# Performance work log

Hardware: AMD Instinct MI355X
Metric: run time of the kernel (lower is better)

## Reference

```python
import jax, jax.numpy as jnp
import numpy as np

# Hard-coded joint groups from GLAGCNModule (num_joints=25)
GROUPS = [
    list(range(25)),                    # full_body
    [0, 1, 2, 3, 4, 5, 6, 7, 8],        # upper_body
    [0, 9, 10, 11, 12, 13, 14],         # lower_body
    [6, 7, 8, 12, 13, 14],              # left_limbs
    [3, 4, 5, 9, 10, 11],               # right_limbs
]

B, N, D_IN, D_HID = 8192, 25, 256, 512


def setup_inputs() -> dict:
    key = jax.random.key(0)
    ks = jax.random.split(key, 7)
    # Xavier-uniform-ish scales for the stacked per-group GCN weights
    s1 = float(np.sqrt(6.0 / (D_IN + D_HID)))
    s2 = float(np.sqrt(6.0 / (D_HID + D_IN)))
    return {
        "x": jax.random.normal(ks[0], (B, N, D_IN), dtype=jnp.float32),
        "adj": jax.random.uniform(ks[1], (B, N, N), dtype=jnp.float32),
        "W1": jax.random.uniform(ks[2], (5, D_IN, D_HID), jnp.float32, -s1, s1),
        "b1": jnp.zeros((5, D_HID), dtype=jnp.float32),
        "W2": jax.random.uniform(ks[3], (5, D_HID, D_IN), jnp.float32, -s2, s2),
        "b2": jnp.zeros((5, D_IN), dtype=jnp.float32),
        "fusion_w": jnp.ones((5,), dtype=jnp.float32),
    }


def _graph_conv(x, adj, W, b):
    """x: (B,n,din), adj: (B,n,n) -> (B,n,dout). Sym-normalized GCN + ReLU."""
    n = adj.shape[-1]
    A = adj + jnp.eye(n, dtype=adj.dtype)          # add self-loops
    deg = jnp.sum(A, axis=-1)                      # (B,n)
    deg_safe = jnp.where(deg == 0, 1.0, deg)
    dinv = jnp.where(deg == 0, 0.0, deg_safe ** -0.5)  # inf -> 0 as in torch
    norm_adj = dinv[:, :, None] * A * dinv[:, None, :]  # D^-1/2 A D^-1/2
    support = jnp.einsum('bnd,de->bne', x, W)
    out = jnp.einsum('bnm,bme->bne', norm_adj, support) + b
    return jax.nn.relu(out)


def reference(x, adj, W1, b1, W2, b2, fusion_w):
    norm_w = jax.nn.softmax(fusion_w)
    fused = jnp.zeros_like(x)
    for g, idx_list in enumerate(GROUPS):
        idx = jnp.asarray(idx_list)
        x_g = x[:, idx, :]                      # (B, ng, D)
        adj_g = adj[:, idx][:, :, idx]          # (B, ng, ng) gather of sub-adjacency
        h = _graph_conv(x_g, adj_g, W1[g], b1[g])
        out_g = _graph_conv(h, adj_g, W2[g], b2[g])
        # scatter back to full joint set, weighted fuse
        fused = fused.at[:, idx, :].add(norm_w[g] * out_g)
    return fused
```

## Files before the change

### kernel.cpp

```cpp
#include <hip/hip_runtime.h>
#include <hip/hip_bf16.h>
#include <stdint.h>

typedef short bf16x8 __attribute__((ext_vector_type(8)));
typedef float f32x4 __attribute__((ext_vector_type(4)));
typedef unsigned short u16;
typedef unsigned int u32;

#define B_TOT 8192
#define NN 25

__device__ __forceinline__ u16 f2bf(float f) {
  u32 u = __float_as_uint(f);
  u32 r = (u + 0x7fffu + ((u >> 16) & 1u)) >> 16;
  return (u16)r;
}
__device__ __forceinline__ float bf2f(u16 h) {
  return __uint_as_float(((u32)h) << 16);
}

__device__ __constant__ int d_IDXT[5][25] = {
  {0,1,2,3,4,5,6,7,8,9,10,11,12,13,14,15,16,17,18,19,20,21,22,23,24},
  {0,1,2,3,4,5,6,7,8, 0,0,0,0,0,0,0,0,0,0,0,0,0,0,0,0},
  {0,9,10,11,12,13,14, 0,0,0,0,0,0,0,0,0,0,0,0,0,0,0,0,0,0},
  {6,7,8,12,13,14, 0,0,0,0,0,0,0,0,0,0,0,0,0,0,0,0,0,0,0},
  {3,4,5,9,10,11, 0,0,0,0,0,0,0,0,0,0,0,0,0,0,0,0,0,0,0}
};
__device__ __constant__ int d_NG[5]    = {25, 9, 7, 6, 6};
__device__ __constant__ int d_BW[5]    = {1, 3, 4, 5, 5};
__device__ __constant__ int d_PREFN[5] = {0, 25, 34, 41, 47};
__device__ __constant__ int d_GCNT[25] = {3,2,2,3,3,3,3,3,3,3,3,3,3,3,3,1,1,1,1,1,1,1,1,1,1};
__device__ __constant__ signed char d_GG[25][3] = {
  {0,1,2},{0,1,0},{0,1,0},{0,1,4},{0,1,4},{0,1,4},{0,1,3},{0,1,3},{0,1,3},
  {0,2,4},{0,2,4},{0,2,4},{0,2,3},{0,2,3},{0,2,3},
  {0,0,0},{0,0,0},{0,0,0},{0,0,0},{0,0,0},{0,0,0},{0,0,0},{0,0,0},{0,0,0},{0,0,0}};
__device__ __constant__ signed char d_GP[25][3] = {
  {0,0,0},{1,1,0},{2,2,0},{3,3,0},{4,4,1},{5,5,2},{6,6,0},{7,7,1},{8,8,2},
  {9,1,3},{10,2,4},{11,3,5},{12,4,3},{13,5,4},{14,6,5},
  {15,0,0},{16,0,0},{17,0,0},{18,0,0},{19,0,0},{20,0,0},{21,0,0},{22,0,0},{23,0,0},{24,0,0}};

__global__ __launch_bounds__(256) void prep_kernel(const float* __restrict__ W1,
                                                   const float* __restrict__ W2,
                                                   u16* __restrict__ w1t,
                                                   u16* __restrict__ w2t) {
  __shared__ float tile[32][33];
  int bid = blockIdx.x, t = threadIdx.x;
  const float* src; u16* dst; int R, C, tr, tc;
  if (bid < 640) {
    int g = bid >> 7, tI = bid & 127;
    R = 256; C = 512; tr = tI >> 4; tc = tI & 15;
    src = W1 + (size_t)g * 131072; dst = w1t + (size_t)g * 131072;
  } else {
    int b2 = bid - 640; int g = b2 >> 7, tI = b2 & 127;
    R = 512; C = 256; tr = tI >> 3; tc = tI & 7;
    src = W2 + (size_t)g * 131072; dst = w2t + (size_t)g * 131072;
  }
  for (int e = t; e < 1024; e += 256) {
    int r = e >> 5, c = e & 31;
    tile[r][c] = src[(size_t)(tr * 32 + r) * C + tc * 32 + c];
  }
  __syncthreads();
  for (int e = t; e < 1024; e += 256) {
    int c = e >> 5, r = e & 31;
    dst[(size_t)(tc * 32 + c) * R + tr * 32 + r] = f2bf(tile[r][c]);
  }
}

struct __align__(16) SMem {
  u16 xs[120 * 256];
  u16 wt[128 * 64];
  u16 bd[128 * 32];
  u16 u[256 * 128];
  float b1s[512];
  float b2s[256];
  float dinv[500];
  u16 rowLUT[128];
};
static_assert(sizeof(SMem) <= 160 * 1024, "LDS overflow");

__global__ __launch_bounds__(512) void gcn_group_kernel(
    const float* __restrict__ x, const float* __restrict__ adj,
    const float* __restrict__ b1, const float* __restrict__ b2,
    const float* __restrict__ fw,
    const u16* __restrict__ w1t, const u16* __restrict__ w2t,
    u16* __restrict__ wsout, float* __restrict__ out, int use_ws) {
  __shared__ SMem sm;
  int bid = blockIdx.x;
  int g, tile;
  if (bid < 2048)      { g = 0; tile = bid; }
  else if (bid < 2731) { g = 1; tile = bid - 2048; }
  else if (bid < 3243) { g = 2; tile = bid - 2731; }
  else if (bid < 3653) { g = 3; tile = bid - 3243; }
  else                 { g = 4; tile = bid - 3653; }
  const int ng = d_NG[g], bw = d_BW[g];
  const int tb = bw * 4;
  const int tb0 = tile * tb;
  const int tid = threadIdx.x;
  const int lane = tid & 63, wid = tid >> 6, wm = wid >> 2, wn = wid & 3;

  if (tid < 128) {
    int w = tid >> 5, off = tid & 31;
    int j = off / ng, i = off - j * ng;
    int valid = (j < bw) ? 1 : 0;
    int bl = w * bw + j;
    sm.rowLUT[tid] = (u16)((valid << 15) | ((bl & 31) << 5) | i);
  }
  sm.b1s[tid] = b1[g * 512 + tid];
  if (tid < 256) sm.b2s[tid] = b2[g * 256 + tid];

  const int nrows = tb * ng;
  for (int cid = tid; cid < nrows * 64; cid += 512) {
    int r = cid >> 6, c4 = cid & 63;
    int bl = r / ng, i = r - bl * ng;
    int b = tb0 + bl;
    float4 v = make_float4(0.f, 0.f, 0.f, 0.f);
    if (b < B_TOT) {
      const float* p = x + ((size_t)b * NN + d_IDXT[g][i]) * 256 + c4 * 4;
      v = *(const float4*)p;
    }
    u32 p0 = (u32)f2bf(v.x) | ((u32)f2bf(v.y) << 16);
    u32 p1 = (u32)f2bf(v.z) | ((u32)f2bf(v.w) << 16);
    u32 off = (u32)r * 512u + (((u32)c4 * 8u) ^ (((u32)r & 7u) << 4));
    *(uint2*)((char*)sm.xs + off) = make_uint2(p0, p1);
  }

  if (tid < nrows) {
    int bl = tid / ng, i = tid - bl * ng;
    int b = tb0 + bl;
    float s = 1.0f;
    if (b < B_TOT) {
      const float* ar = adj + ((size_t)b * NN + d_IDXT[g][i]) * NN;
      for (int j2 = 0; j2 < ng; ++j2) s += ar[d_IDXT[g][j2]];
    }
    sm.dinv[bl * 25 + i] = (s > 0.f) ? rsqrtf(s) : 0.f;
  }
  __syncthreads();

  u32 arow[4], aswz[4];
#pragma unroll
  for (int m = 0; m < 4; ++m) {
    int r = wm * 64 + m * 16 + (lane & 15);
    u16 lut = sm.rowLUT[r];
    int rxs = 0;
    if (lut & 0x8000) rxs = ((lut >> 5) & 31) * ng + (lut & 31);
    arow[m] = (u32)rxs * 512u;
    aswz[m] = ((u32)rxs & 7u) << 4;
  }

  for (int e = tid; e < 4096; e += 512) {
    int r = e >> 5, c = e & 31;
    u16 lr = sm.rowLUT[r];
    u16 lc = sm.rowLUT[(r & ~31) | c];
    float val = 0.f;
    int blr = (lr >> 5) & 31, ir = lr & 31;
    int blc = (lc >> 5) & 31, ic = lc & 31;
    int b = tb0 + blr;
    if ((lr >> 15) && (lc >> 15) && blr == blc && b < B_TOT) {
      float a = adj[((size_t)b * NN + d_IDXT[g][ir]) * NN + d_IDXT[g][ic]] +
                (ir == ic ? 1.f : 0.f);
      val = sm.dinv[blr * 25 + ir] * a * sm.dinv[blr * 25 + ic];
    }
    u32 off = (u32)r * 64u + (((u32)c * 2u) ^ (((u32)r & 3u) << 4));
    *(u16*)((char*)sm.bd + off) = f2bf(val);
  }

  float wg = 0.2f;
  if (!use_ws) {
    float a0 = fw[0], a1 = fw[1], a2 = fw[2], a3 = fw[3], a4 = fw[4];
    float mx = fmaxf(fmaxf(fmaxf(a0, a1), fmaxf(a2, a3)), a4);
    float e0 = __expf(a0 - mx), e1 = __expf(a1 - mx), e2 = __expf(a2 - mx),
          e3 = __expf(a3 - mx), e4 = __expf(a4 - mx);
    float es[5] = {e0, e1, e2, e3, e4};
    wg = es[g] / (e0 + e1 + e2 + e3 + e4);
  }

  f32x4 zero4 = {0.f, 0.f, 0.f, 0.f};
  f32x4 accO[4][2][2];
#pragma unroll
  for (int m = 0; m < 4; ++m)
#pragma unroll
    for (int a = 0; a < 2; ++a)
#pragma unroll
      for (int bq = 0; bq < 2; ++bq) accO[m][a][bq] = zero4;

#pragma unroll 1
  for (int c = 0; c < 4; ++c) {
    f32x4 accS[4][2];
#pragma unroll
    for (int m = 0; m < 4; ++m) { accS[m][0] = zero4; accS[m][1] = zero4; }

    for (int kt = 0; kt < 4; ++kt) {
#pragma unroll
      for (int it = 0; it < 2; ++it) {
        int cid = tid + it * 512;
        int row = cid >> 3, p = cid & 7;
        const u16* src = w1t + (size_t)(g * 512 + c * 128 + row) * 256 + kt * 64 + p * 8;
        uint4 v = *(const uint4*)src;
        u32 off = (u32)row * 128u + (((u32)p * 16u) ^ (((u32)row & 7u) << 4));
        *(uint4*)((char*)sm.wt + off) = v;
      }
      __syncthreads();
#pragma unroll
      for (int ks = 0; ks < 2; ++ks) {
        u32 colb = (u32)(kt * 128 + ks * 64) + (((u32)lane >> 4) << 4);
        bf16x8 afr[4];
#pragma unroll
        for (int m = 0; m < 4; ++m)
          afr[m] = *(const bf16x8*)((const char*)sm.xs + arow[m] + (colb ^ aswz[m]));
#pragma unroll
        for (int nf = 0; nf < 2; ++nf) {
          int nl = (wn * 2 + nf) * 16 + (lane & 15);
          u32 boff = (u32)nl * 128u +
                     (((u32)(ks * 64) + (((u32)lane >> 4) << 4)) ^ (((u32)nl & 7u) << 4));
          bf16x8 bfr = *(const bf16x8*)((const char*)sm.wt + boff);
#pragma unroll
          for (int m = 0; m < 4; ++m)
            accS[m][nf] = __builtin_amdgcn_mfma_f32_16x16x32_bf16(afr[m], bfr, accS[m][nf], 0, 0, 0);
        }
      }
      __syncthreads();
    }

#pragma unroll
    for (int m = 0; m < 4; ++m) {
      int mrow0 = wm * 64 + m * 16 + ((lane >> 4) << 2);
#pragma unroll
      for (int nf = 0; nf < 2; ++nf) {
        int f = (wn * 2 + nf) * 16 + (lane & 15);
        u32 p0 = (u32)f2bf(accS[m][nf][0]) | ((u32)f2bf(accS[m][nf][1]) << 16);
        u32 p1 = (u32)f2bf(accS[m][nf][2]) | ((u32)f2bf(accS[m][nf][3]) << 16);
        u32 off = (u32)f * 256u + (((u32)mrow0 * 2u) ^ (((u32)f & 7u) << 4));
        *(uint2*)((char*)sm.u + off) = make_uint2(p0, p1);
      }
    }
    __syncthreads();

#pragma unroll
    for (int m = 0; m < 4; ++m) {
      int mf = wm * 4 + m, win = mf >> 1;
      int br = mf * 16 + (lane & 15);
      u32 aoff = (u32)br * 64u + (((((u32)lane >> 4) << 4)) ^ (((u32)br & 3u) << 4));
      bf16x8 abd = *(const bf16x8*)((const char*)sm.bd + aoff);
#pragma unroll
      for (int nf = 0; nf < 2; ++nf) {
        int f = (wn * 2 + nf) * 16 + (lane & 15);
        u32 boff = (u32)f * 256u +
                   (((u32)(win * 64) + (((u32)lane >> 4) << 4)) ^ (((u32)f & 7u) << 4));
        bf16x8 bfr = *(const bf16x8*)((const char*)sm.u + boff);
        f32x4 d = zero4;
        d = __builtin_amdgcn_mfma_f32_16x16x32_bf16(abd, bfr, d, 0, 0, 0);
        float bb = sm.b1s[c * 128 + f];
#pragma unroll
        for (int r2 = 0; r2 < 4; ++r2) {
          int mrow = mf * 16 + ((lane >> 4) << 2) + r2;
          float hv = d[r2] + bb;
          hv = hv > 0.f ? hv : 0.f;
          u32 hoff = 32768u + (u32)mrow * 256u + (((u32)f * 2u) ^ (((u32)mrow & 7u) << 4));
          *(u16*)((char*)sm.u + hoff) = f2bf(hv);
        }
      }
    }
    __syncthreads();

#pragma unroll
    for (int nh = 0; nh < 2; ++nh) {
#pragma unroll
      for (int kt2 = 0; kt2 < 2; ++kt2) {
#pragma unroll
        for (int it = 0; it < 2; ++it) {
          int cid = tid + it * 512;
          int row = cid >> 3, p = cid & 7;
          const u16* src = w2t + (size_t)(g * 256 + nh * 128 + row) * 512 +
                           c * 128 + kt2 * 64 + p * 8;
          uint4 v = *(const uint4*)src;
          u32 off = (u32)row * 128u + (((u32)p * 16u) ^ (((u32)row & 7u) << 4));
          *(uint4*)((char*)sm.wt + off) = v;
        }
        __syncthreads();
#pragma unroll
        for (int ks = 0; ks < 2; ++ks) {
          bf16x8 afr[4];
#pragma unroll
          for (int m = 0; m < 4; ++m) {
            int mrow = wm * 64 + m * 16 + (lane & 15);
            u32 aoff = 32768u + (u32)mrow * 256u +
                       (((u32)(kt2 * 128 + ks * 64) + (((u32)lane >> 4) << 4)) ^
                        (((u32)mrow & 7u) << 4));
            afr[m] = *(const bf16x8*)((const char*)sm.u + aoff);
          }
#pragma unroll
          for (int nf = 0; nf < 2; ++nf) {
            int nl = (wn * 2 + nf) * 16 + (lane & 15);
            u32 boff = (u32)nl * 128u +
                       (((u32)(ks * 64) + (((u32)lane >> 4) << 4)) ^ (((u32)nl & 7u) << 4));
            bf16x8 bfr = *(const bf16x8*)((const char*)sm.wt + boff);
#pragma unroll
            for (int m = 0; m < 4; ++m)
              accO[m][nh][nf] =
                  __builtin_amdgcn_mfma_f32_16x16x32_bf16(afr[m], bfr, accO[m][nh][nf], 0, 0, 0);
          }
        }
        __syncthreads();
      }
    }
  }

#pragma unroll
  for (int m = 0; m < 4; ++m) {
    int mrow0 = wm * 64 + m * 16 + ((lane >> 4) << 2);
#pragma unroll
    for (int nh = 0; nh < 2; ++nh)
#pragma unroll
      for (int nf = 0; nf < 2; ++nf) {
        int f = nh * 128 + (wn * 2 + nf) * 16 + (lane & 15);
        u32 p0 = (u32)f2bf(accO[m][nh][nf][0]) | ((u32)f2bf(accO[m][nh][nf][1]) << 16);
        u32 p1 = (u32)f2bf(accO[m][nh][nf][2]) | ((u32)f2bf(accO[m][nh][nf][3]) << 16);
        u32 off = (u32)f * 256u + (((u32)mrow0 * 2u) ^ (((u32)f & 7u) << 4));
        *(uint2*)((char*)sm.u + off) = make_uint2(p0, p1);
      }
  }
  __syncthreads();

  u16* wbase = wsout + (size_t)d_PREFN[g] * B_TOT * 256;
#pragma unroll
  for (int m = 0; m < 4; ++m) {
    int mf = wm * 4 + m, win = mf >> 1;
    int br = mf * 16 + (lane & 15);
    u32 aoff = (u32)br * 64u + (((((u32)lane >> 4) << 4)) ^ (((u32)br & 3u) << 4));
    bf16x8 abd = *(const bf16x8*)((const char*)sm.bd + aoff);
#pragma unroll
    for (int q = 0; q < 4; ++q) {
      int f = (wn * 4 + q) * 16 + (lane & 15);
      u32 boff = (u32)f * 256u +
                 (((u32)(win * 64) + (((u32)lane >> 4) << 4)) ^ (((u32)f & 7u) << 4));
      bf16x8 bfr = *(const bf16x8*)((const char*)sm.u + boff);
      f32x4 d = zero4;
      d = __builtin_amdgcn_mfma_f32_16x16x32_bf16(abd, bfr, d, 0, 0, 0);
      float bb = sm.b2s[f];
#pragma unroll
      for (int r2 = 0; r2 < 4; ++r2) {
        int mrow = mf * 16 + ((lane >> 4) << 2) + r2;
        u16 lut = sm.rowLUT[mrow];
        if (!(lut & 0x8000)) continue;
        int bl = (lut >> 5) & 31, i = lut & 31;
        int b = tb0 + bl;
        if (b >= B_TOT) continue;
        float v = d[r2] + bb;
        v = v > 0.f ? v : 0.f;
        if (use_ws) {
          wbase[((size_t)b * ng + i) * 256 + f] = f2bf(v);
        } else {
          float* dst = out + ((size_t)b * NN + d_IDXT[g][i]) * 256 + f;
          __hip_atomic_fetch_add(dst, wg * v, __ATOMIC_RELAXED, __HIP_MEMORY_SCOPE_AGENT);
        }
      }
    }
  }
}

__global__ __launch_bounds__(256) void gather_kernel(const u16* __restrict__ wsout,
                                                     const float* __restrict__ fw,
                                                     float* __restrict__ out) {
  int t = blockIdx.x * 256 + threadIdx.x;
  int b = t / 1600;
  int rem = t - b * 1600;
  int v = rem >> 6;
  int f = (rem & 63) << 2;
  float a0 = fw[0], a1 = fw[1], a2 = fw[2], a3 = fw[3], a4 = fw[4];
  float mx = fmaxf(fmaxf(fmaxf(a0, a1), fmaxf(a2, a3)), a4);
  float e0 = __expf(a0 - mx), e1 = __expf(a1 - mx), e2 = __expf(a2 - mx),
        e3 = __expf(a3 - mx), e4 = __expf(a4 - mx);
  float inv = 1.f / (e0 + e1 + e2 + e3 + e4);
  float w[5] = {e0 * inv, e1 * inv, e2 * inv, e3 * inv, e4 * inv};
  float acc0 = 0.f, acc1 = 0.f, acc2 = 0.f, acc3 = 0.f;
  int cnt = d_GCNT[v];
  for (int k = 0; k < cnt; ++k) {
    int g = d_GG[v][k], pos = d_GP[v][k];
    const u16* p = wsout + (size_t)d_PREFN[g] * B_TOT * 256 +
                   ((size_t)b * d_NG[g] + pos) * 256 + f;
    ushort4 h = *(const ushort4*)p;
    float ww = w[g];
    acc0 += ww * bf2f(h.x);
    acc1 += ww * bf2f(h.y);
    acc2 += ww * bf2f(h.z);
    acc3 += ww * bf2f(h.w);
  }
  *(float4*)(out + (size_t)t * 4) = make_float4(acc0, acc1, acc2, acc3);
}

extern "C" void kernel_launch(void* const* d_in, const int* in_sizes, int n_in,
                              void* d_out, int out_size, void* d_ws, size_t ws_size,
                              hipStream_t stream) {
  const float* x   = (const float*)d_in[0];
  const float* adj = (const float*)d_in[1];
  const float* W1  = (const float*)d_in[2];
  const float* b1  = (const float*)d_in[3];
  const float* W2  = (const float*)d_in[4];
  const float* b2  = (const float*)d_in[5];
  const float* fw  = (const float*)d_in[6];
  float* out = (float*)d_out;
  char* ws = (char*)d_ws;

  u16* w1t   = (u16*)ws;
  u16* w2t   = (u16*)(ws + 1310720);
  u16* wsout = (u16*)(ws + 2621440);
  const size_t need = 2621440ull + 53ull * 8192ull * 256ull * 2ull;
  const int use_ws = (ws_size >= need) ? 1 : 0;

  prep_kernel<<<1280, 256, 0, stream>>>(W1, W2, w1t, w2t);
  if (!use_ws) {
    hipMemsetAsync(out, 0, (size_t)out_size * sizeof(float), stream);
  }
  gcn_group_kernel<<<4063, 512, 0, stream>>>(x, adj, b1, b2, fw, w1t, w2t,
                                             wsout, out, use_ws);
  if (use_ws) {
    gather_kernel<<<51200, 256, 0, stream>>>(wsout, fw, out);
  }
}
```

Baseline: 1.500 ms.

## Load GEMM weight fragments straight from global memory and transpose the adjacency MFMA epilogue

Removes the shared-memory weight tile and the per-k-step barriers. Each lane now loads its W1/W2 bf16 fragments directly from global memory (expected to hit L2) into registers. The block-diagonal adjacency MFMAs are transposed so each lane holds four consecutive features of a single row. This lets bias loads, h stores and output writes be vectorized (float4/uint2), with the row LUT checked once per row. The trade is more global and L2 load traffic and register pressure in exchange for fewer syncs and less LDS use.

```diff
diff --git a/kernel.cpp b/kernel.cpp
--- a/kernel.cpp
+++ b/kernel.cpp
@@ -68,7 +68,6 @@
 
 struct __align__(16) SMem {
   u16 xs[120 * 256];
-  u16 wt[128 * 64];
   u16 bd[128 * 32];
   u16 u[256 * 128];
   float b1s[512];
@@ -183,23 +182,25 @@
 #pragma unroll
       for (int bq = 0; bq < 2; ++bq) accO[m][a][bq] = zero4;
 
+  __syncthreads();
+
 #pragma unroll 1
   for (int c = 0; c < 4; ++c) {
     f32x4 accS[4][2];
 #pragma unroll
     for (int m = 0; m < 4; ++m) { accS[m][0] = zero4; accS[m][1] = zero4; }
 
+#pragma unroll
     for (int kt = 0; kt < 4; ++kt) {
-#pragma unroll
-      for (int it = 0; it < 2; ++it) {
-        int cid = tid + it * 512;
-        int row = cid >> 3, p = cid & 7;
-        const u16* src = w1t + (size_t)(g * 512 + c * 128 + row) * 256 + kt * 64 + p * 8;
-        uint4 v = *(const uint4*)src;
-        u32 off = (u32)row * 128u + (((u32)p * 16u) ^ (((u32)row & 7u) << 4));
-        *(uint4*)((char*)sm.wt + off) = v;
-      }
-      __syncthreads();
+      bf16x8 bfr[2][2];
+#pragma unroll
+      for (int ks = 0; ks < 2; ++ks)
+#pragma unroll
+        for (int nf = 0; nf < 2; ++nf) {
+          int n = c * 128 + (wn * 2 + nf) * 16 + (lane & 15);
+          int k = kt * 64 + ks * 32 + ((lane >> 4) << 3);
+          bfr[ks][nf] = *(const bf16x8*)(w1t + ((size_t)(g * 512 + n) * 256 + k));
+        }
 #pragma unroll
       for (int ks = 0; ks < 2; ++ks) {
         u32 colb = (u32)(kt * 128 + ks * 64) + (((u32)lane >> 4) << 4);
@@ -208,17 +209,11 @@
         for (int m = 0; m < 4; ++m)
           afr[m] = *(const bf16x8*)((const char*)sm.xs + arow[m] + (colb ^ aswz[m]));
 #pragma unroll
-        for (int nf = 0; nf < 2; ++nf) {
-          int nl = (wn * 2 + nf) * 16 + (lane & 15);
-          u32 boff = (u32)nl * 128u +
-                     (((u32)(ks * 64) + (((u32)lane >> 4) << 4)) ^ (((u32)nl & 7u) << 4));
-          bf16x8 bfr = *(const bf16x8*)((const char*)sm.wt + boff);
+        for (int nf = 0; nf < 2; ++nf)
 #pragma unroll
           for (int m = 0; m < 4; ++m)
-            accS[m][nf] = __builtin_amdgcn_mfma_f32_16x16x32_bf16(afr[m], bfr, accS[m][nf], 0, 0, 0);
-        }
-      }
-      __syncthreads();
+            accS[m][nf] = __builtin_amdgcn_mfma_f32_16x16x32_bf16(afr[m], bfr[ks][nf], accS[m][nf], 0, 0, 0);
+      }
     }
 
 #pragma unroll
@@ -237,46 +232,44 @@
 
 #pragma unroll
     for (int m = 0; m < 4; ++m) {
-      int mf = wm * 4 + m, win = mf >> 1;
-      int br = mf * 16 + (lane & 15);
-      u32 aoff = (u32)br * 64u + (((((u32)lane >> 4) << 4)) ^ (((u32)br & 3u) << 4));
-      bf16x8 abd = *(const bf16x8*)((const char*)sm.bd + aoff);
-#pragma unroll
-      for (int nf = 0; nf < 2; ++nf) {
-        int f = (wn * 2 + nf) * 16 + (lane & 15);
-        u32 boff = (u32)f * 256u +
+      int mb = wm * 4 + m, win = mb >> 1;
+      int mrow = mb * 16 + (lane & 15);
+      u32 boff = (u32)mrow * 64u + (((((u32)lane >> 4) << 4)) ^ (((u32)mrow & 3u) << 4));
+      bf16x8 bfr = *(const bf16x8*)((const char*)sm.bd + boff);
+#pragma unroll
+      for (int a = 0; a < 2; ++a) {
+        int f = (wn * 2 + a) * 16 + (lane & 15);
+        u32 aoff = (u32)f * 256u +
                    (((u32)(win * 64) + (((u32)lane >> 4) << 4)) ^ (((u32)f & 7u) << 4));
-        bf16x8 bfr = *(const bf16x8*)((const char*)sm.u + boff);
-        f32x4 d = zero4;
-        d = __builtin_amdgcn_mfma_f32_16x16x32_bf16(abd, bfr, d, 0, 0, 0);
-        float bb = sm.b1s[c * 128 + f];
-#pragma unroll
-        for (int r2 = 0; r2 < 4; ++r2) {
-          int mrow = mf * 16 + ((lane >> 4) << 2) + r2;
-          float hv = d[r2] + bb;
-          hv = hv > 0.f ? hv : 0.f;
-          u32 hoff = 32768u + (u32)mrow * 256u + (((u32)f * 2u) ^ (((u32)mrow & 7u) << 4));
-          *(u16*)((char*)sm.u + hoff) = f2bf(hv);
-        }
+        bf16x8 afr = *(const bf16x8*)((const char*)sm.u + aoff);
+        f32x4 d = __builtin_amdgcn_mfma_f32_16x16x32_bf16(afr, bfr, zero4, 0, 0, 0);
+        int f0 = (wn * 2 + a) * 16 + ((lane >> 4) << 2);
+        float4 bb = *(const float4*)&sm.b1s[c * 128 + f0];
+        float h0 = d[0] + bb.x; h0 = h0 > 0.f ? h0 : 0.f;
+        float h1 = d[1] + bb.y; h1 = h1 > 0.f ? h1 : 0.f;
+        float h2 = d[2] + bb.z; h2 = h2 > 0.f ? h2 : 0.f;
+        float h3 = d[3] + bb.w; h3 = h3 > 0.f ? h3 : 0.f;
+        u32 p0 = (u32)f2bf(h0) | ((u32)f2bf(h1) << 16);
+        u32 p1 = (u32)f2bf(h2) | ((u32)f2bf(h3) << 16);
+        u32 hoff = 32768u + (u32)mrow * 256u + (((u32)f0 * 2u) ^ (((u32)mrow & 7u) << 4));
+        *(uint2*)((char*)sm.u + hoff) = make_uint2(p0, p1);
       }
     }
     __syncthreads();
 
 #pragma unroll
-    for (int nh = 0; nh < 2; ++nh) {
+    for (int nh = 0; nh < 2; ++nh)
 #pragma unroll
       for (int kt2 = 0; kt2 < 2; ++kt2) {
-#pragma unroll
-        for (int it = 0; it < 2; ++it) {
-          int cid = tid + it * 512;
-          int row = cid >> 3, p = cid & 7;
-          const u16* src = w2t + (size_t)(g * 256 + nh * 128 + row) * 512 +
-                           c * 128 + kt2 * 64 + p * 8;
-          uint4 v = *(const uint4*)src;
-          u32 off = (u32)row * 128u + (((u32)p * 16u) ^ (((u32)row & 7u) << 4));
-          *(uint4*)((char*)sm.wt + off) = v;
-        }
-        __syncthreads();
+        bf16x8 bfr2[2][2];
+#pragma unroll
+        for (int ks = 0; ks < 2; ++ks)
+#pragma unroll
+          for (int nf = 0; nf < 2; ++nf) {
+            int n = nh * 128 + (wn * 2 + nf) * 16 + (lane & 15);
+            int k = c * 128 + kt2 * 64 + ks * 32 + ((lane >> 4) << 3);
+            bfr2[ks][nf] = *(const bf16x8*)(w2t + ((size_t)(g * 256 + n) * 512 + k));
+          }
 #pragma unroll
         for (int ks = 0; ks < 2; ++ks) {
           bf16x8 afr[4];
@@ -289,21 +282,16 @@
             afr[m] = *(const bf16x8*)((const char*)sm.u + aoff);
           }
 #pragma unroll
-          for (int nf = 0; nf < 2; ++nf) {
-            int nl = (wn * 2 + nf) * 16 + (lane & 15);
-            u32 boff = (u32)nl * 128u +
-                       (((u32)(ks * 64) + (((u32)lane >> 4) << 4)) ^ (((u32)nl & 7u) << 4));
-            bf16x8 bfr = *(const bf16x8*)((const char*)sm.wt + boff);
+          for (int nf = 0; nf < 2; ++nf)
 #pragma unroll
             for (int m = 0; m < 4; ++m)
               accO[m][nh][nf] =
-                  __builtin_amdgcn_mfma_f32_16x16x32_bf16(afr[m], bfr, accO[m][nh][nf], 0, 0, 0);
-          }
+                  __builtin_amdgcn_mfma_f32_16x16x32_bf16(afr[m], bfr2[ks][nf], accO[m][nh][nf], 0, 0, 0);
         }
-        __syncthreads();
-      }
-    }
-  }
+      }
+  }
+
+  __syncthreads();
 
 #pragma unroll
   for (int m = 0; m < 4; ++m) {
@@ -324,34 +312,39 @@
   u16* wbase = wsout + (size_t)d_PREFN[g] * B_TOT * 256;
 #pragma unroll
   for (int m = 0; m < 4; ++m) {
-    int mf = wm * 4 + m, win = mf >> 1;
-    int br = mf * 16 + (lane & 15);
-    u32 aoff = (u32)br * 64u + (((((u32)lane >> 4) << 4)) ^ (((u32)br & 3u) << 4));
-    bf16x8 abd = *(const bf16x8*)((const char*)sm.bd + aoff);
+    int mb = wm * 4 + m, win = mb >> 1;
+    int mrow = mb * 16 + (lane & 15);
+    u32 boff = (u32)mrow * 64u + (((((u32)lane >> 4) << 4)) ^ (((u32)mrow & 3u) << 4));
+    bf16x8 bfr = *(const bf16x8*)((const char*)sm.bd + boff);
+    u16 lut = sm.rowLUT[mrow];
+    int bl = (lut >> 5) & 31, i = lut & 31;
+    int b = tb0 + bl;
+    bool ok = (lut & 0x8000) && (b < B_TOT);
 #pragma unroll
     for (int q = 0; q < 4; ++q) {
-      int f = (wn * 4 + q) * 16 + (lane & 15);
-      u32 boff = (u32)f * 256u +
+      int fb = wn * 4 + q;
+      int f = fb * 16 + (lane & 15);
+      u32 aoff = (u32)f * 256u +
                  (((u32)(win * 64) + (((u32)lane >> 4) << 4)) ^ (((u32)f & 7u) << 4));
-      bf16x8 bfr = *(const bf16x8*)((const char*)sm.u + boff);
-      f32x4 d = zero4;
-      d = __builtin_amdgcn_mfma_f32_16x16x32_bf16(abd, bfr, d, 0, 0, 0);
-      float bb = sm.b2s[f];
-#pragma unroll
-      for (int r2 = 0; r2 < 4; ++r2) {
-        int mrow = mf * 16 + ((lane >> 4) << 2) + r2;
-        u16 lut = sm.rowLUT[mrow];
-        if (!(lut & 0x8000)) continue;
-        int bl = (lut >> 5) & 31, i = lut & 31;
-        int b = tb0 + bl;
-        if (b >= B_TOT) continue;
-        float v = d[r2] + bb;
-        v = v > 0.f ? v : 0.f;
+      bf16x8 afr = *(const bf16x8*)((const char*)sm.u + aoff);
+      f32x4 d = __builtin_amdgcn_mfma_f32_16x16x32_bf16(afr, bfr, zero4, 0, 0, 0);
+      int f0 = fb * 16 + ((lane >> 4) << 2);
+      float4 bb = *(const float4*)&sm.b2s[f0];
+      float v0 = d[0] + bb.x; v0 = v0 > 0.f ? v0 : 0.f;
+      float v1 = d[1] + bb.y; v1 = v1 > 0.f ? v1 : 0.f;
+      float v2 = d[2] + bb.z; v2 = v2 > 0.f ? v2 : 0.f;
+      float v3 = d[3] + bb.w; v3 = v3 > 0.f ? v3 : 0.f;
+      if (ok) {
         if (use_ws) {
-          wbase[((size_t)b * ng + i) * 256 + f] = f2bf(v);
+          u32 p0 = (u32)f2bf(v0) | ((u32)f2bf(v1) << 16);
+          u32 p1 = (u32)f2bf(v2) | ((u32)f2bf(v3) << 16);
+          *(uint2*)(wbase + ((size_t)b * ng + i) * 256 + f0) = make_uint2(p0, p1);
         } else {
-          float* dst = out + ((size_t)b * NN + d_IDXT[g][i]) * 256 + f;
-          __hip_atomic_fetch_add(dst, wg * v, __ATOMIC_RELAXED, __HIP_MEMORY_SCOPE_AGENT);
+          float* dst = out + ((size_t)b * NN + d_IDXT[g][i]) * 256 + f0;
+          __hip_atomic_fetch_add(dst + 0, wg * v0, __ATOMIC_RELAXED, __HIP_MEMORY_SCOPE_AGENT);
+          __hip_atomic_fetch_add(dst + 1, wg * v1, __ATOMIC_RELAXED, __HIP_MEMORY_SCOPE_AGENT);
+          __hip_atomic_fetch_add(dst + 2, wg * v2, __ATOMIC_RELAXED, __HIP_MEMORY_SCOPE_AGENT);
+          __hip_atomic_fetch_add(dst + 3, wg * v3, __ATOMIC_RELAXED, __HIP_MEMORY_SCOPE_AGENT);
         }
       }
     }
```

Result: faster. 1.423 ms (-5.1%).
